# Performance work log

Measured on AMD Instinct MI355X. Metric: run time of the kernel, lower is better.

## Reference

```python
import jax, jax.numpy as jnp
import numpy as np


def setup_inputs() -> dict:
    key = jax.random.key(0)
    B, N = 256, 512
    # binary symmetric-ish adjacency (0/1 entries)
    adj = jax.random.randint(key, (B, N, N), 0, 2).astype(jnp.float32)
    return {"adjacency": adj}


def reference(adjacency):
    # atom mask: rows with any connection
    atom_mask = (jnp.sum(adjacency, axis=-1) != 0).astype(adjacency.dtype)  # [B, N]
    N = adjacency.shape[-1]
    eye = jnp.eye(N, dtype=adjacency.dtype)
    # set_diag(adjacency, atom_mask): zero existing diagonal, insert mask
    adjacency_hat = adjacency * (1.0 - eye) + eye * atom_mask[..., :, None]
    degree_hat = jnp.sum(adjacency_hat, axis=-1)  # [B, N]
    d_sqrt = jnp.sqrt(degree_hat)
    # reciprocal_no_nan: 1/x where x != 0, else 0
    d_inv_sqrt = jnp.where(d_sqrt == 0, 0.0, 1.0 / jnp.where(d_sqrt == 0, 1.0, d_sqrt))
    # D^-1/2 A_hat D^-1/2 as row/column scaling (equivalent to the diag matmuls)
    adjacency_norm = d_inv_sqrt[..., :, None] * adjacency_hat * d_inv_sqrt[..., None, :]
    return adjacency_norm
```

## Files before the change

kernel.cpp:

```cpp
#include <hip/hip_runtime.h>
#include <hip/hip_bf16.h>


#define NN 512
#define NB 256

typedef float f32x4 __attribute__((ext_vector_type(4)));

__global__ __launch_bounds__(256) void degree_compress_kernel(
    const float* __restrict__ adj, float* __restrict__ dinv,
    unsigned char* __restrict__ cmp) {
    int gtid = blockIdx.x * blockDim.x + threadIdx.x;
    int row  = gtid >> 6;
    int lane = threadIdx.x & 63;

    const f32x4* r4 = (const f32x4*)(adj + (size_t)row * NN);
    f32x4 a0 = __builtin_nontemporal_load(&r4[lane]);
    f32x4 a1 = __builtin_nontemporal_load(&r4[lane + 64]);

    float s = (a0.x + a0.y) + (a0.z + a0.w) + (a1.x + a1.y) + (a1.z + a1.w);

    unsigned nib0 = (a0.x != 0.0f ? 1u : 0u) | (a0.y != 0.0f ? 2u : 0u)
                  | (a0.z != 0.0f ? 4u : 0u) | (a0.w != 0.0f ? 8u : 0u);
    unsigned nib1 = (a1.x != 0.0f ? 1u : 0u) | (a1.y != 0.0f ? 2u : 0u)
                  | (a1.z != 0.0f ? 4u : 0u) | (a1.w != 0.0f ? 8u : 0u);
    cmp[(size_t)row * 64 + lane] = (unsigned char)(nib0 | (nib1 << 4));

    int i = row & (NN - 1);
    float diag = 0.0f;
    int j0 = lane << 2;
    if (i >= j0 && i < j0 + 4) diag = ((const float*)&a0)[i - j0];
    int j1 = 256 + (lane << 2);
    if (i >= j1 && i < j1 + 4) diag = ((const float*)&a1)[i - j1];

    #pragma unroll
    for (int off = 32; off > 0; off >>= 1) {
        s    += __shfl_xor(s, off);
        diag += __shfl_xor(diag, off);
    }

    if (lane == 0) {
        float mask = (s != 0.0f) ? 1.0f : 0.0f;
        float deg  = s - diag + mask;
        dinv[row]  = (deg > 0.0f) ? (1.0f / sqrtf(deg)) : 0.0f;
    }
}

#define RPW 8
__global__ __launch_bounds__(256) void expand_kernel(
    const unsigned char* __restrict__ cmp, const float* __restrict__ dinv,
    float* __restrict__ out) {
    const int lane  = threadIdx.x & 63;
    const int waveg = (blockIdx.x << 2) | (threadIdx.x >> 6);
    size_t row0 = (size_t)waveg * RPW;

    const int j0 = lane << 2;
    const int j1 = 256 + (lane << 2);

    for (int rr = 0; rr < RPW; ++rr) {
        const size_t row  = row0 + rr;
        const size_t rowb = row & ~(size_t)(NN - 1);
        const int    i    = (int)(row & (NN - 1));

        unsigned bits = cmp[row * 64 + lane];

        if ((i >> 2) == lane && i < 256)              bits |= 1u << (i & 3);
        if (((i - 256) >> 2) == lane && i >= 256)     bits |= 1u << (4 + (i & 3));

        const float di  = dinv[row];
        const f32x4 dj0 = ((const f32x4*)(dinv + rowb))[lane];
        const f32x4 dj1 = ((const f32x4*)(dinv + rowb))[lane + 64];

        f32x4 o0, o1;
        o0.x = (bits &   1u) ? di * dj0.x : 0.0f;
        o0.y = (bits &   2u) ? di * dj0.y : 0.0f;
        o0.z = (bits &   4u) ? di * dj0.z : 0.0f;
        o0.w = (bits &   8u) ? di * dj0.w : 0.0f;
        o1.x = (bits &  16u) ? di * dj1.x : 0.0f;
        o1.y = (bits &  32u) ? di * dj1.y : 0.0f;
        o1.z = (bits &  64u) ? di * dj1.z : 0.0f;
        o1.w = (bits & 128u) ? di * dj1.w : 0.0f;

        f32x4* dst = (f32x4*)(out + row * NN);
        __builtin_nontemporal_store(o0, &dst[lane]);
        __builtin_nontemporal_store(o1, &dst[lane + 64]);
    }
}

extern "C" void kernel_launch(void* const* d_in, const int* in_sizes, int n_in,
                              void* d_out, int out_size, void* d_ws, size_t ws_size,
                              hipStream_t stream) {
    const float* adj = (const float*)d_in[0];
    float* out  = (float*)d_out;
    float* dinv = (float*)d_ws;
    unsigned char* cmp = (unsigned char*)d_ws + (1u << 20);

    const int totalRows = NB * NN;
    degree_compress_kernel<<<totalRows / 4, 256, 0, stream>>>(adj, dinv, cmp);

    const int nblk = totalRows / (RPW * 4);
    expand_kernel<<<nblk, 256, 0, stream>>>(cmp, dinv, out);
}
```

Before: 418.5 us.

## Fuse degree computation and expansion into one per-batch kernel using shared memory

Replaces the two-kernel pipeline with a single kernel where each 1024-thread block handles one batch matrix. Row bitmasks and inverse-sqrt degrees are kept in shared memory instead of a global workspace, which removes a launch and the workspace round trip. The row-sum and diagonal reductions are packed into one shuffle reduction by encoding them as 2*s+diag, which relies on integer-valued entries. This costs occupancy (one large block per CU) and forces a barrier between the read phase and the write phase.

```diff
diff --git a/kernel.cpp b/kernel.cpp
--- a/kernel.cpp
+++ b/kernel.cpp
@@ -1,5 +1,4 @@
 #include <hip/hip_runtime.h>
-#include <hip/hip_bf16.h>
 
 
 #define NN 512
@@ -7,81 +6,76 @@
 
 typedef float f32x4 __attribute__((ext_vector_type(4)));
 
-__global__ __launch_bounds__(256) void degree_compress_kernel(
-    const float* __restrict__ adj, float* __restrict__ dinv,
-    unsigned char* __restrict__ cmp) {
-    int gtid = blockIdx.x * blockDim.x + threadIdx.x;
-    int row  = gtid >> 6;
-    int lane = threadIdx.x & 63;
+__global__ __launch_bounds__(1024) void fused_norm_kernel(
+    const float* __restrict__ adj, float* __restrict__ out) {
+    __shared__ unsigned char sbits[NN][64];
+    __shared__ float sdinv[NN];
 
-    const f32x4* r4 = (const f32x4*)(adj + (size_t)row * NN);
-    f32x4 a0 = __builtin_nontemporal_load(&r4[lane]);
-    f32x4 a1 = __builtin_nontemporal_load(&r4[lane + 64]);
+    const int lane = threadIdx.x & 63;
+    const int wave = threadIdx.x >> 6;
+    const size_t base = (size_t)blockIdx.x * ((size_t)NN * NN);
 
-    float s = (a0.x + a0.y) + (a0.z + a0.w) + (a1.x + a1.y) + (a1.z + a1.w);
+    #pragma unroll 4
+    for (int rr = 0; rr < 32; ++rr) {
+        const int i = (wave << 5) + rr;
+        const f32x4* r4 = (const f32x4*)(adj + base + (size_t)i * NN);
+        f32x4 a0 = __builtin_nontemporal_load(&r4[lane]);
+        f32x4 a1 = __builtin_nontemporal_load(&r4[lane + 64]);
 
-    unsigned nib0 = (a0.x != 0.0f ? 1u : 0u) | (a0.y != 0.0f ? 2u : 0u)
-                  | (a0.z != 0.0f ? 4u : 0u) | (a0.w != 0.0f ? 8u : 0u);
-    unsigned nib1 = (a1.x != 0.0f ? 1u : 0u) | (a1.y != 0.0f ? 2u : 0u)
-                  | (a1.z != 0.0f ? 4u : 0u) | (a1.w != 0.0f ? 8u : 0u);
-    cmp[(size_t)row * 64 + lane] = (unsigned char)(nib0 | (nib1 << 4));
+        float s = (a0.x + a0.y) + (a0.z + a0.w) + (a1.x + a1.y) + (a1.z + a1.w);
 
-    int i = row & (NN - 1);
-    float diag = 0.0f;
-    int j0 = lane << 2;
-    if (i >= j0 && i < j0 + 4) diag = ((const float*)&a0)[i - j0];
-    int j1 = 256 + (lane << 2);
-    if (i >= j1 && i < j1 + 4) diag = ((const float*)&a1)[i - j1];
+        unsigned nib0 = (a0.x != 0.0f ? 1u : 0u) | (a0.y != 0.0f ? 2u : 0u)
+                      | (a0.z != 0.0f ? 4u : 0u) | (a0.w != 0.0f ? 8u : 0u);
+        unsigned nib1 = (a1.x != 0.0f ? 1u : 0u) | (a1.y != 0.0f ? 2u : 0u)
+                      | (a1.z != 0.0f ? 4u : 0u) | (a1.w != 0.0f ? 8u : 0u);
+        unsigned byte = nib0 | (nib1 << 4);
 
-    #pragma unroll
-    for (int off = 32; off > 0; off >>= 1) {
-        s    += __shfl_xor(s, off);
-        diag += __shfl_xor(diag, off);
+        float diag = 0.0f;
+        const int j0 = lane << 2;
+        if (i >= j0 && i < j0 + 4) diag = ((const float*)&a0)[i - j0];
+        const int j1 = 256 + j0;
+        if (i >= j1 && i < j1 + 4) diag = ((const float*)&a1)[i - j1];
+
+        if ((i >> 2) == lane)                       byte |= 1u << (i & 3);
+        if (i >= 256 && ((i - 256) >> 2) == lane)   byte |= 1u << (4 + (i & 3));
+
+        sbits[i][lane] = (unsigned char)byte;
+
+        float t = s + s + diag;
+        #pragma unroll
+        for (int off = 32; off > 0; off >>= 1) t += __shfl_xor(t, off);
+
+        if (lane == 0) {
+            float S = floorf(t * 0.5f);
+            float D = t - (S + S);
+            float mask = (S != 0.0f) ? 1.0f : 0.0f;
+            float deg  = S - D + mask;
+            sdinv[i] = (deg > 0.0f) ? (1.0f / sqrtf(deg)) : 0.0f;
+        }
     }
 
-    if (lane == 0) {
-        float mask = (s != 0.0f) ? 1.0f : 0.0f;
-        float deg  = s - diag + mask;
-        dinv[row]  = (deg > 0.0f) ? (1.0f / sqrtf(deg)) : 0.0f;
-    }
-}
+    __syncthreads();
 
-#define RPW 8
-__global__ __launch_bounds__(256) void expand_kernel(
-    const unsigned char* __restrict__ cmp, const float* __restrict__ dinv,
-    float* __restrict__ out) {
-    const int lane  = threadIdx.x & 63;
-    const int waveg = (blockIdx.x << 2) | (threadIdx.x >> 6);
-    size_t row0 = (size_t)waveg * RPW;
+    const f32x4 dj0 = ((const f32x4*)sdinv)[lane];
+    const f32x4 dj1 = ((const f32x4*)sdinv)[lane + 64];
 
-    const int j0 = lane << 2;
-    const int j1 = 256 + (lane << 2);
-
-    for (int rr = 0; rr < RPW; ++rr) {
-        const size_t row  = row0 + rr;
-        const size_t rowb = row & ~(size_t)(NN - 1);
-        const int    i    = (int)(row & (NN - 1));
-
-        unsigned bits = cmp[row * 64 + lane];
-
-        if ((i >> 2) == lane && i < 256)              bits |= 1u << (i & 3);
-        if (((i - 256) >> 2) == lane && i >= 256)     bits |= 1u << (4 + (i & 3));
-
-        const float di  = dinv[row];
-        const f32x4 dj0 = ((const f32x4*)(dinv + rowb))[lane];
-        const f32x4 dj1 = ((const f32x4*)(dinv + rowb))[lane + 64];
+    #pragma unroll 2
+    for (int rr = 0; rr < 32; ++rr) {
+        const int i = (wave << 5) + rr;
+        const unsigned bb = sbits[i][lane];
+        const float di = sdinv[i];
 
         f32x4 o0, o1;
-        o0.x = (bits &   1u) ? di * dj0.x : 0.0f;
-        o0.y = (bits &   2u) ? di * dj0.y : 0.0f;
-        o0.z = (bits &   4u) ? di * dj0.z : 0.0f;
-        o0.w = (bits &   8u) ? di * dj0.w : 0.0f;
-        o1.x = (bits &  16u) ? di * dj1.x : 0.0f;
-        o1.y = (bits &  32u) ? di * dj1.y : 0.0f;
-        o1.z = (bits &  64u) ? di * dj1.z : 0.0f;
-        o1.w = (bits & 128u) ? di * dj1.w : 0.0f;
+        o0.x = (bb &   1u) ? di * dj0.x : 0.0f;
+        o0.y = (bb &   2u) ? di * dj0.y : 0.0f;
+        o0.z = (bb &   4u) ? di * dj0.z : 0.0f;
+        o0.w = (bb &   8u) ? di * dj0.w : 0.0f;
+        o1.x = (bb &  16u) ? di * dj1.x : 0.0f;
+        o1.y = (bb &  32u) ? di * dj1.y : 0.0f;
+        o1.z = (bb &  64u) ? di * dj1.z : 0.0f;
+        o1.w = (bb & 128u) ? di * dj1.w : 0.0f;
 
-        f32x4* dst = (f32x4*)(out + row * NN);
+        f32x4* dst = (f32x4*)(out + base + (size_t)i * NN);
         __builtin_nontemporal_store(o0, &dst[lane]);
         __builtin_nontemporal_store(o1, &dst[lane + 64]);
     }
@@ -91,13 +85,7 @@
                               void* d_out, int out_size, void* d_ws, size_t ws_size,
                               hipStream_t stream) {
     const float* adj = (const float*)d_in[0];
-    float* out  = (float*)d_out;
-    float* dinv = (float*)d_ws;
-    unsigned char* cmp = (unsigned char*)d_ws + (1u << 20);
-
-    const int totalRows = NB * NN;
-    degree_compress_kernel<<<totalRows / 4, 256, 0, stream>>>(adj, dinv, cmp);
-
-    const int nblk = totalRows / (RPW * 4);
-    expand_kernel<<<nblk, 256, 0, stream>>>(cmp, dinv, out);
+    float* out = (float*)d_out;
+    (void)d_ws; (void)ws_size;
+    fused_norm_kernel<<<NB, 1024, 0, stream>>>(adj, out);
 }
```

After: 411.0 us. About the same (-1.8%).
